# Performance work log

Measured on AMD Instinct MI355X. Metric: run time of the kernel, lower is better.

Reference implementation:

```python
import jax, jax.numpy as jnp
import numpy as np

B, W, Q = 64, 128, 256
H, A, C = 512, 128, 20
SCALE = 0.05  # keep gates out of saturation


def setup_inputs() -> dict:
    key = jax.random.key(0)
    ks = jax.random.split(key, 9)
    return {
        "quantized_repr": jax.random.normal(ks[0], (B, W, Q), jnp.float32),
        "w_in": jax.random.normal(ks[1], (H, Q), jnp.float32) * SCALE,
        "b_in": jax.random.normal(ks[2], (H,), jnp.float32) * SCALE,
        "w_ih": jax.random.normal(ks[3], (4 * H, A), jnp.float32) * SCALE,
        "w_hh": jax.random.normal(ks[4], (4 * H, H), jnp.float32) * SCALE,
        "b_ih": jax.random.normal(ks[5], (4 * H,), jnp.float32) * SCALE,
        "b_hh": jax.random.normal(ks[6], (4 * H,), jnp.float32) * SCALE,
        "w_out": jax.random.normal(ks[7], (A, H), jnp.float32) * SCALE,
        "b_out": jax.random.normal(ks[8], (A,), jnp.float32) * SCALE,
        "max_char_len": C,
    }


def reference(quantized_repr, w_in, b_in, w_ih, w_hh, b_ih, b_hh, w_out, b_out, max_char_len):
    b, w, q = quantized_repr.shape
    hdim = w_hh.shape[1]
    vocab = w_out.shape[0]
    dt = quantized_repr.dtype

    # input_projection -> initial hidden, zero cell, flattened over (B*W)
    h0 = (quantized_repr @ w_in.T + b_in).reshape(b * w, hdim)
    c0 = jnp.zeros_like(h0)
    x0 = jax.nn.one_hot(jnp.zeros((b * w,), jnp.int32), vocab, dtype=dt)  # <start> = char 0
    bias = b_ih + b_hh

    def step(carry, _):
        h, c, x = carry
        gates = x @ w_ih.T + h @ w_hh.T + bias  # [BW, 4H]
        i, f, g, o = jnp.split(gates, 4, axis=-1)  # torch gate order i,f,g,o
        i = jax.nn.sigmoid(i)
        f = jax.nn.sigmoid(f)
        g = jnp.tanh(g)
        o = jax.nn.sigmoid(o)
        c = f * c + i * g
        h = o * jnp.tanh(c)
        logits = h @ w_out.T + b_out  # [BW, A]
        x_next = jax.nn.one_hot(jnp.argmax(logits, axis=-1), vocab, dtype=dt)
        return (h, c, x_next), logits

    _, logits = jax.lax.scan(step, (h0, c0, x0), None, length=max_char_len)  # [C, BW, A]
    return logits.transpose(1, 0, 2).reshape(b, w, max_char_len, vocab)
```

## Files before the change

kernel.cpp:

```cpp
#include <hip/hip_runtime.h>
#include <math.h>

typedef float fv4 __attribute__((ext_vector_type(4)));

#define NSTEP 20
#define HD 512
#define QD 256
#define VOC 128
#define RB 16
#define TPB 512
#define CREG 2
#define CLDSROWS (RB - CREG)

#define WG_OFF   0
#define WIH_OFF  1048576
#define WIN_OFF  1310720
#define WOUT_OFF 1441792

__device__ __forceinline__ float sig_np(float x) {
  float t = (float)exp(-(double)x);
  return __fdiv_rn(1.0f, __fadd_rn(1.0f, t));
}
__device__ __forceinline__ float tanh_np(float x) {
  return (float)tanh((double)x);
}

__global__ void repack_kernel(const float* __restrict__ w_in,
                              const float* __restrict__ w_ih,
                              const float* __restrict__ w_hh,
                              const float* __restrict__ w_out,
                              float* __restrict__ ws) {
  int t = blockIdx.x * blockDim.x + threadIdx.x;
  {
    int ki = t & 3, u = (t >> 2) & 511, g = (t >> 11) & 3, kb = t >> 13;
    ws[WG_OFF + t] = w_hh[(size_t)(g * HD + u) * HD + kb * 4 + ki];
  }
  if (t < 262144) {
    int u = t & 511, g = (t >> 9) & 3, x = t >> 11;
    ws[WIH_OFF + t] = w_ih[(size_t)(g * HD + u) * VOC + x];
  }
  if (t < 131072) {
    int ki = t & 3, u = (t >> 2) & 511, kb = t >> 11;
    ws[WIN_OFF + t] = w_in[(size_t)u * QD + kb * 4 + ki];
  }
  if (t < 65536) {
    int ki = t & 3, v = (t >> 2) & 127, kb = t >> 9;
    ws[WOUT_OFF + t] = w_out[(size_t)v * HD + kb * 4 + ki];
  }
}

__global__ __launch_bounds__(TPB, 2)
void decoder_fast(const float* __restrict__ quant,
                  const float* __restrict__ b_in,
                  const float* __restrict__ b_ih,
                  const float* __restrict__ b_hh,
                  const float* __restrict__ b_out,
                  const float* __restrict__ ws,
                  float* __restrict__ out) {
  __shared__ __align__(16) float hLDS[RB * HD];
  __shared__ __align__(16) float cLDS[CLDSROWS * HD];
  __shared__ float2 cand[RB][2];

  const int tid  = threadIdx.x;
  const int row0 = blockIdx.x * RB;
  const int v    = tid & (VOC - 1);
  const int rqs  = (tid >> 7) << 2;
  const int wpar = (tid >> 6) & 1;

  const fv4* Wg4   = (const fv4*)(ws + WG_OFF);
  const float* Wih = ws + WIH_OFF;
  const fv4* Win4  = (const fv4*)(ws + WIN_OFF);
  const fv4* Wout4 = (const fv4*)(ws + WOUT_OFF);
  const fv4* hLDS4 = (const fv4*)hLDS;

  {
    const fv4* src = (const fv4*)(quant + (size_t)row0 * QD);
    fv4* dst = (fv4*)hLDS;
    dst[tid]       = src[tid];
    dst[tid + TPB] = src[tid + TPB];
  }
  __syncthreads();

  float a0[RB];
  {
    const fv4* q4 = (const fv4*)hLDS;
#pragma unroll
    for (int r = 0; r < RB; ++r) a0[r] = 0.0f;
    for (int kb = 0; kb < QD / 4; ++kb) {
      fv4 w = Win4[kb * 512 + tid];
#pragma unroll
      for (int r = 0; r < RB; ++r) {
        fv4 qv = q4[r * 64 + kb];
        a0[r] = __builtin_fmaf(w[0], qv[0], a0[r]);
        a0[r] = __builtin_fmaf(w[1], qv[1], a0[r]);
        a0[r] = __builtin_fmaf(w[2], qv[2], a0[r]);
        a0[r] = __builtin_fmaf(w[3], qv[3], a0[r]);
      }
    }
  }
  const float binu = b_in[tid];
  __syncthreads();
#pragma unroll
  for (int r = 0; r < RB; ++r) hLDS[r * HD + tid] = __fadd_rn(a0[r], binu);
  __syncthreads();

  float cR0 = 0.0f, cR1 = 0.0f;

  for (int t = 0; t < NSTEP; ++t) {
    float acc[RB][4];
    float la[4];
#pragma unroll
    for (int rr = 0; rr < RB; ++rr)
#pragma unroll
      for (int g = 0; g < 4; ++g) acc[rr][g] = 0.0f;
#pragma unroll
    for (int j = 0; j < 4; ++j) la[j] = 0.0f;

    for (int kb = 0; kb < HD / 4; ++kb) {
      fv4 wv[4];
#pragma unroll
      for (int g = 0; g < 4; ++g) wv[g] = Wg4[(kb * 4 + g) * 512 + tid];
      fv4 wvo = Wout4[kb * 128 + v];
#pragma unroll
      for (int rr = 0; rr < RB; ++rr) {
        const int r = (rr + rqs) & (RB - 1);
        fv4 hv = hLDS4[r * 128 + kb];
#pragma unroll
        for (int g = 0; g < 4; ++g) {
          acc[rr][g] = __builtin_fmaf(wv[g][0], hv[0], acc[rr][g]);
          acc[rr][g] = __builtin_fmaf(wv[g][1], hv[1], acc[rr][g]);
          acc[rr][g] = __builtin_fmaf(wv[g][2], hv[2], acc[rr][g]);
          acc[rr][g] = __builtin_fmaf(wv[g][3], hv[3], acc[rr][g]);
        }
        if (rr < 4) {
          la[rr] = __builtin_fmaf(wvo[0], hv[0], la[rr]);
          la[rr] = __builtin_fmaf(wvo[1], hv[1], la[rr]);
          la[rr] = __builtin_fmaf(wvo[2], hv[2], la[rr]);
          la[rr] = __builtin_fmaf(wvo[3], hv[3], la[rr]);
        }
      }
    }

    if (t > 0) {
      const float boutv = b_out[v];
#pragma unroll
      for (int j = 0; j < 4; ++j) {
        float val = __fadd_rn(la[j], boutv);
        out[(size_t)((row0 + rqs + j) * NSTEP + (t - 1)) * VOC + v] = val;
        float mv = val;
        int   mi = v;
#pragma unroll
        for (int m = 1; m < 64; m <<= 1) {
          float ov = __shfl_xor(mv, m);
          int   oi = __shfl_xor(mi, m);
          bool take = (ov > mv) || (ov == mv && oi < mi);
          mv = take ? ov : mv;
          mi = take ? oi : mi;
        }
        if ((tid & 63) == 0)
          cand[rqs + j][wpar] = make_float2(mv, __int_as_float(mi));
      }
    }
    __syncthreads();

    float biasg[4];
#pragma unroll
    for (int g = 0; g < 4; ++g)
      biasg[g] = __fadd_rn(b_ih[g * HD + tid], b_hh[g * HD + tid]);

#pragma unroll
    for (int rr = 0; rr < RB; ++rr) {
      const int r = (rr + rqs) & (RB - 1);
      int ix = 0;
      if (t > 0) {
        float2 c0 = cand[r][0], c1 = cand[r][1];
        ix = (c1.x > c0.x) ? __float_as_int(c1.y) : __float_as_int(c0.y);
      }
      float ga[4];
#pragma unroll
      for (int g = 0; g < 4; ++g) {
        float t1 = Wih[(ix * 4 + g) * 512 + tid];
        ga[g] = __fadd_rn(__fadd_rn(t1, acc[rr][g]), biasg[g]);
      }
      float ig = sig_np(ga[0]);
      float fg = sig_np(ga[1]);
      float gg = tanh_np(ga[2]);
      float og = sig_np(ga[3]);
      float cold;
      if (rr == RB - 2)      cold = cR0;
      else if (rr == RB - 1) cold = cR1;
      else                   cold = cLDS[rr * HD + tid];
      if (t == 0) cold = 0.0f;
      float cn = __fadd_rn(__fmul_rn(fg, cold), __fmul_rn(ig, gg));
      if (rr == RB - 2)      cR0 = cn;
      else if (rr == RB - 1) cR1 = cn;
      else                   cLDS[rr * HD + tid] = cn;
      hLDS[r * HD + tid] = __fmul_rn(og, tanh_np(cn));
    }
    __syncthreads();
  }

  {
    float la2[4];
#pragma unroll
    for (int j = 0; j < 4; ++j) la2[j] = 0.0f;
    for (int kb = 0; kb < HD / 4; ++kb) {
      fv4 wvo = Wout4[kb * 128 + v];
#pragma unroll
      for (int j = 0; j < 4; ++j) {
        fv4 hv = hLDS4[(rqs + j) * 128 + kb];
        la2[j] = __builtin_fmaf(wvo[0], hv[0], la2[j]);
        la2[j] = __builtin_fmaf(wvo[1], hv[1], la2[j]);
        la2[j] = __builtin_fmaf(wvo[2], hv[2], la2[j]);
        la2[j] = __builtin_fmaf(wvo[3], hv[3], la2[j]);
      }
    }
    const float boutv = b_out[v];
#pragma unroll
    for (int j = 0; j < 4; ++j)
      out[(size_t)((row0 + rqs + j) * NSTEP + (NSTEP - 1)) * VOC + v] =
          __fadd_rn(la2[j], boutv);
  }
}

extern "C" void kernel_launch(void* const* d_in, const int* in_sizes, int n_in,
                              void* d_out, int out_size, void* d_ws, size_t ws_size,
                              hipStream_t stream) {
  const float* quant = (const float*)d_in[0];
  const float* w_in  = (const float*)d_in[1];
  const float* b_in  = (const float*)d_in[2];
  const float* w_ih  = (const float*)d_in[3];
  const float* w_hh  = (const float*)d_in[4];
  const float* b_ih  = (const float*)d_in[5];
  const float* b_hh  = (const float*)d_in[6];
  const float* w_out = (const float*)d_in[7];
  const float* b_out = (const float*)d_in[8];
  float* out = (float*)d_out;
  float* ws  = (float*)d_ws;

  repack_kernel<<<4096, 256, 0, stream>>>(w_in, w_ih, w_hh, w_out, ws);
  decoder_fast<<<8192 / RB, TPB, 0, stream>>>(quant, b_in, b_ih, b_hh, b_out,
                                              ws, out);
}
```

Before: 5.993 ms.

## Halve rows per block, keep cell state in registers, interleave gate weights

Cuts rows per block from 16 to 8, which doubles the block count and raises the launch-bounds occupancy target from 2 to 4. The cell state moves from LDS plus two registers into a register array. The repack now interleaves the four gates per unit so each thread loads its gate weights and its W_ih row as contiguous vectors, and bias loads are hoisted out of the time loop. The cost is half the reuse of each streamed w_hh weight per block, so total weight traffic from global memory/L2 doubles in exchange for more parallelism and latency hiding.

```diff
diff --git a/kernel.cpp b/kernel.cpp
--- a/kernel.cpp
+++ b/kernel.cpp
@@ -7,10 +7,8 @@
 #define HD 512
 #define QD 256
 #define VOC 128
-#define RB 16
+#define RB 8
 #define TPB 512
-#define CREG 2
-#define CLDSROWS (RB - CREG)
 
 #define WG_OFF   0
 #define WIH_OFF  1048576
@@ -32,11 +30,11 @@
                               float* __restrict__ ws) {
   int t = blockIdx.x * blockDim.x + threadIdx.x;
   {
-    int ki = t & 3, u = (t >> 2) & 511, g = (t >> 11) & 3, kb = t >> 13;
+    int ki = t & 3, g = (t >> 2) & 3, u = (t >> 4) & 511, kb = t >> 13;
     ws[WG_OFF + t] = w_hh[(size_t)(g * HD + u) * HD + kb * 4 + ki];
   }
   if (t < 262144) {
-    int u = t & 511, g = (t >> 9) & 3, x = t >> 11;
+    int g = t & 3, u = (t >> 2) & 511, x = t >> 11;
     ws[WIH_OFF + t] = w_ih[(size_t)(g * HD + u) * VOC + x];
   }
   if (t < 131072) {
@@ -49,7 +47,7 @@
   }
 }
 
-__global__ __launch_bounds__(TPB, 2)
+__global__ __launch_bounds__(TPB, 4)
 void decoder_fast(const float* __restrict__ quant,
                   const float* __restrict__ b_in,
                   const float* __restrict__ b_ih,
@@ -58,13 +56,12 @@
                   const float* __restrict__ ws,
                   float* __restrict__ out) {
   __shared__ __align__(16) float hLDS[RB * HD];
-  __shared__ __align__(16) float cLDS[CLDSROWS * HD];
   __shared__ float2 cand[RB][2];
 
   const int tid  = threadIdx.x;
   const int row0 = blockIdx.x * RB;
   const int v    = tid & (VOC - 1);
-  const int rqs  = (tid >> 7) << 2;
+  const int rqs  = (tid >> 7) << 1;
   const int wpar = (tid >> 6) & 1;
 
   const fv4* Wg4   = (const fv4*)(ws + WG_OFF);
@@ -75,9 +72,7 @@
 
   {
     const fv4* src = (const fv4*)(quant + (size_t)row0 * QD);
-    fv4* dst = (fv4*)hLDS;
-    dst[tid]       = src[tid];
-    dst[tid + TPB] = src[tid + TPB];
+    ((fv4*)hLDS)[tid] = src[tid];
   }
   __syncthreads();
 
@@ -102,24 +97,34 @@
   __syncthreads();
 #pragma unroll
   for (int r = 0; r < RB; ++r) hLDS[r * HD + tid] = __fadd_rn(a0[r], binu);
+
+  float biasg[4];
+#pragma unroll
+  for (int g = 0; g < 4; ++g)
+    biasg[g] = __fadd_rn(b_ih[g * HD + tid], b_hh[g * HD + tid]);
+  const float boutv = b_out[v];
+
+  float c[RB];
+#pragma unroll
+  for (int r = 0; r < RB; ++r) c[r] = 0.0f;
+
   __syncthreads();
-
-  float cR0 = 0.0f, cR1 = 0.0f;
 
   for (int t = 0; t < NSTEP; ++t) {
     float acc[RB][4];
-    float la[4];
+    float la[2];
 #pragma unroll
     for (int rr = 0; rr < RB; ++rr)
 #pragma unroll
       for (int g = 0; g < 4; ++g) acc[rr][g] = 0.0f;
 #pragma unroll
-    for (int j = 0; j < 4; ++j) la[j] = 0.0f;
+    for (int j = 0; j < 2; ++j) la[j] = 0.0f;
 
     for (int kb = 0; kb < HD / 4; ++kb) {
+      const fv4* wp = Wg4 + ((size_t)kb << 11) + (tid << 2);
       fv4 wv[4];
 #pragma unroll
-      for (int g = 0; g < 4; ++g) wv[g] = Wg4[(kb * 4 + g) * 512 + tid];
+      for (int g = 0; g < 4; ++g) wv[g] = wp[g];
       fv4 wvo = Wout4[kb * 128 + v];
 #pragma unroll
       for (int rr = 0; rr < RB; ++rr) {
@@ -132,7 +137,7 @@
           acc[rr][g] = __builtin_fmaf(wv[g][2], hv[2], acc[rr][g]);
           acc[rr][g] = __builtin_fmaf(wv[g][3], hv[3], acc[rr][g]);
         }
-        if (rr < 4) {
+        if (rr < 2) {
           la[rr] = __builtin_fmaf(wvo[0], hv[0], la[rr]);
           la[rr] = __builtin_fmaf(wvo[1], hv[1], la[rr]);
           la[rr] = __builtin_fmaf(wvo[2], hv[2], la[rr]);
@@ -142,9 +147,8 @@
     }
 
     if (t > 0) {
-      const float boutv = b_out[v];
-#pragma unroll
-      for (int j = 0; j < 4; ++j) {
+#pragma unroll
+      for (int j = 0; j < 2; ++j) {
         float val = __fadd_rn(la[j], boutv);
         out[(size_t)((row0 + rqs + j) * NSTEP + (t - 1)) * VOC + v] = val;
         float mv = val;
@@ -163,11 +167,6 @@
     }
     __syncthreads();
 
-    float biasg[4];
-#pragma unroll
-    for (int g = 0; g < 4; ++g)
-      biasg[g] = __fadd_rn(b_ih[g * HD + tid], b_hh[g * HD + tid]);
-
 #pragma unroll
     for (int rr = 0; rr < RB; ++rr) {
       const int r = (rr + rqs) & (RB - 1);
@@ -176,38 +175,30 @@
         float2 c0 = cand[r][0], c1 = cand[r][1];
         ix = (c1.x > c0.x) ? __float_as_int(c1.y) : __float_as_int(c0.y);
       }
+      fv4 t4 = *(const fv4*)&Wih[((size_t)ix << 11) + (tid << 2)];
       float ga[4];
 #pragma unroll
-      for (int g = 0; g < 4; ++g) {
-        float t1 = Wih[(ix * 4 + g) * 512 + tid];
-        ga[g] = __fadd_rn(__fadd_rn(t1, acc[rr][g]), biasg[g]);
-      }
+      for (int g = 0; g < 4; ++g)
+        ga[g] = __fadd_rn(__fadd_rn(t4[g], acc[rr][g]), biasg[g]);
       float ig = sig_np(ga[0]);
       float fg = sig_np(ga[1]);
       float gg = tanh_np(ga[2]);
       float og = sig_np(ga[3]);
-      float cold;
-      if (rr == RB - 2)      cold = cR0;
-      else if (rr == RB - 1) cold = cR1;
-      else                   cold = cLDS[rr * HD + tid];
-      if (t == 0) cold = 0.0f;
-      float cn = __fadd_rn(__fmul_rn(fg, cold), __fmul_rn(ig, gg));
-      if (rr == RB - 2)      cR0 = cn;
-      else if (rr == RB - 1) cR1 = cn;
-      else                   cLDS[rr * HD + tid] = cn;
+      float cn = __fadd_rn(__fmul_rn(fg, c[rr]), __fmul_rn(ig, gg));
+      c[rr] = cn;
       hLDS[r * HD + tid] = __fmul_rn(og, tanh_np(cn));
     }
     __syncthreads();
   }
 
   {
-    float la2[4];
-#pragma unroll
-    for (int j = 0; j < 4; ++j) la2[j] = 0.0f;
+    float la2[2];
+#pragma unroll
+    for (int j = 0; j < 2; ++j) la2[j] = 0.0f;
     for (int kb = 0; kb < HD / 4; ++kb) {
       fv4 wvo = Wout4[kb * 128 + v];
 #pragma unroll
-      for (int j = 0; j < 4; ++j) {
+      for (int j = 0; j < 2; ++j) {
         fv4 hv = hLDS4[(rqs + j) * 128 + kb];
         la2[j] = __builtin_fmaf(wvo[0], hv[0], la2[j]);
         la2[j] = __builtin_fmaf(wvo[1], hv[1], la2[j]);
@@ -215,9 +206,8 @@
         la2[j] = __builtin_fmaf(wvo[3], hv[3], la2[j]);
       }
     }
-    const float boutv = b_out[v];
-#pragma unroll
-    for (int j = 0; j < 4; ++j)
+#pragma unroll
+    for (int j = 0; j < 2; ++j)
       out[(size_t)((row0 + rqs + j) * NSTEP + (NSTEP - 1)) * VOC + v] =
           __fadd_rn(la2[j], boutv);
   }
```

Result: slower. 6.876 ms (+14.7%).

## Double-buffer LSTM weight loads and interleave gate weights per unit

Applied to the files above, without the earlier changes.

Repacks the recurrent weights so each thread's four gate vectors sit next to each other, and does the same for the input-to-hidden table so one 16-byte load covers all four gates. The k-loop is software-pipelined with two register buffers: the next k-block's weights are prefetched while FMAs run on the current block. Bias loads are hoisted out of the time loop. This targets global-load latency and instruction count, but the extra register buffers may raise VGPR pressure at two blocks per CU.

```diff
diff --git a/kernel.cpp b/kernel.cpp
--- a/kernel.cpp
+++ b/kernel.cpp
@@ -32,11 +32,11 @@
                               float* __restrict__ ws) {
   int t = blockIdx.x * blockDim.x + threadIdx.x;
   {
-    int ki = t & 3, u = (t >> 2) & 511, g = (t >> 11) & 3, kb = t >> 13;
+    int ki = t & 3, g = (t >> 2) & 3, u = (t >> 4) & 511, kb = t >> 13;
     ws[WG_OFF + t] = w_hh[(size_t)(g * HD + u) * HD + kb * 4 + ki];
   }
   if (t < 262144) {
-    int u = t & 511, g = (t >> 9) & 3, x = t >> 11;
+    int g = t & 3, u = (t >> 2) & 511, x = t >> 11;
     ws[WIH_OFF + t] = w_ih[(size_t)(g * HD + u) * VOC + x];
   }
   if (t < 131072) {
@@ -102,9 +102,16 @@
   __syncthreads();
 #pragma unroll
   for (int r = 0; r < RB; ++r) hLDS[r * HD + tid] = __fadd_rn(a0[r], binu);
+
+  float biasg[4];
+#pragma unroll
+  for (int g = 0; g < 4; ++g)
+    biasg[g] = __fadd_rn(b_ih[g * HD + tid], b_hh[g * HD + tid]);
+  const float boutv = b_out[v];
+
+  float cR0 = 0.0f, cR1 = 0.0f;
+
   __syncthreads();
-
-  float cR0 = 0.0f, cR1 = 0.0f;
 
   for (int t = 0; t < NSTEP; ++t) {
     float acc[RB][4];
@@ -116,33 +123,56 @@
 #pragma unroll
     for (int j = 0; j < 4; ++j) la[j] = 0.0f;
 
-    for (int kb = 0; kb < HD / 4; ++kb) {
-      fv4 wv[4];
-#pragma unroll
-      for (int g = 0; g < 4; ++g) wv[g] = Wg4[(kb * 4 + g) * 512 + tid];
-      fv4 wvo = Wout4[kb * 128 + v];
-#pragma unroll
-      for (int rr = 0; rr < RB; ++rr) {
-        const int r = (rr + rqs) & (RB - 1);
-        fv4 hv = hLDS4[r * 128 + kb];
-#pragma unroll
-        for (int g = 0; g < 4; ++g) {
-          acc[rr][g] = __builtin_fmaf(wv[g][0], hv[0], acc[rr][g]);
-          acc[rr][g] = __builtin_fmaf(wv[g][1], hv[1], acc[rr][g]);
-          acc[rr][g] = __builtin_fmaf(wv[g][2], hv[2], acc[rr][g]);
-          acc[rr][g] = __builtin_fmaf(wv[g][3], hv[3], acc[rr][g]);
-        }
-        if (rr < 4) {
-          la[rr] = __builtin_fmaf(wvo[0], hv[0], la[rr]);
-          la[rr] = __builtin_fmaf(wvo[1], hv[1], la[rr]);
-          la[rr] = __builtin_fmaf(wvo[2], hv[2], la[rr]);
-          la[rr] = __builtin_fmaf(wvo[3], hv[3], la[rr]);
-        }
-      }
-    }
+    fv4 wvA[4], wvB[4], wvoA, wvoB;
+    {
+      const fv4* wp = Wg4 + (tid << 2);
+#pragma unroll
+      for (int g = 0; g < 4; ++g) wvA[g] = wp[g];
+      wvoA = Wout4[v];
+    }
+
+#define DO_FMA(KB, WV, WVO)                                              \
+    {                                                                    \
+      _Pragma("unroll")                                                  \
+      for (int rr = 0; rr < RB; ++rr) {                                  \
+        const int r = (rr + rqs) & (RB - 1); \
+        fv4 hv = hLDS4[r * 128 + (KB)];                                  \
+        _Pragma("unroll")                                                \
+        for (int g = 0; g < 4; ++g) {                                    \
+          acc[rr][g] = __builtin_fmaf(WV[g][0], hv[0], acc[rr][g]);      \
+          acc[rr][g] = __builtin_fmaf(WV[g][1], hv[1], acc[rr][g]);      \
+          acc[rr][g] = __builtin_fmaf(WV[g][2], hv[2], acc[rr][g]);      \
+          acc[rr][g] = __builtin_fmaf(WV[g][3], hv[3], acc[rr][g]);      \
+        }                                                                \
+        if (rr < 4) { \
+          la[rr] = __builtin_fmaf(WVO[0], hv[0], la[rr]);                \
+          la[rr] = __builtin_fmaf(WVO[1], hv[1], la[rr]);                \
+          la[rr] = __builtin_fmaf(WVO[2], hv[2], la[rr]);                \
+          la[rr] = __builtin_fmaf(WVO[3], hv[3], la[rr]);                \
+        }                                                                \
+      }                                                                  \
+    }
+
+    for (int kb = 0; kb < HD / 4; kb += 2) {
+      {
+        const fv4* wp = Wg4 + ((size_t)(kb + 1) << 11) + (tid << 2);
+#pragma unroll
+        for (int g = 0; g < 4; ++g) wvB[g] = wp[g];
+        wvoB = Wout4[(kb + 1) * 128 + v];
+      }
+      DO_FMA(kb, wvA, wvoA);
+      {
+        const int kn = (kb + 2) & 127;
+        const fv4* wp = Wg4 + ((size_t)kn << 11) + (tid << 2);
+#pragma unroll
+        for (int g = 0; g < 4; ++g) wvA[g] = wp[g];
+        wvoA = Wout4[kn * 128 + v];
+      }
+      DO_FMA(kb + 1, wvB, wvoB);
+    }
+#undef DO_FMA
 
     if (t > 0) {
-      const float boutv = b_out[v];
 #pragma unroll
       for (int j = 0; j < 4; ++j) {
         float val = __fadd_rn(la[j], boutv);
@@ -163,11 +193,6 @@
     }
     __syncthreads();
 
-    float biasg[4];
-#pragma unroll
-    for (int g = 0; g < 4; ++g)
-      biasg[g] = __fadd_rn(b_ih[g * HD + tid], b_hh[g * HD + tid]);
-
 #pragma unroll
     for (int rr = 0; rr < RB; ++rr) {
       const int r = (rr + rqs) & (RB - 1);
@@ -176,12 +201,11 @@
         float2 c0 = cand[r][0], c1 = cand[r][1];
         ix = (c1.x > c0.x) ? __float_as_int(c1.y) : __float_as_int(c0.y);
       }
+      fv4 t4 = *(const fv4*)&Wih[((size_t)ix << 11) + (tid << 2)];
       float ga[4];
 #pragma unroll
-      for (int g = 0; g < 4; ++g) {
-        float t1 = Wih[(ix * 4 + g) * 512 + tid];
-        ga[g] = __fadd_rn(__fadd_rn(t1, acc[rr][g]), biasg[g]);
-      }
+      for (int g = 0; g < 4; ++g)
+        ga[g] = __fadd_rn(__fadd_rn(t4[g], acc[rr][g]), biasg[g]);
       float ig = sig_np(ga[0]);
       float fg = sig_np(ga[1]);
       float gg = tanh_np(ga[2]);
@@ -215,7 +239,6 @@
         la2[j] = __builtin_fmaf(wvo[3], hv[3], la2[j]);
       }
     }
-    const float boutv = b_out[v];
 #pragma unroll
     for (int j = 0; j < 4; ++j)
       out[(size_t)((row0 + rqs + j) * NSTEP + (NSTEP - 1)) * VOC + v] =
@@ -227,8 +250,8 @@
                               void* d_out, int out_size, void* d_ws, size_t ws_size,
                               hipStream_t stream) {
   const float* quant = (const float*)d_in[0];
+  const float* b_in  = (const float*)d_in[2];
   const float* w_in  = (const float*)d_in[1];
-  const float* b_in  = (const float*)d_in[2];
   const float* w_ih  = (const float*)d_in[3];
   const float* w_hh  = (const float*)d_in[4];
   const float* b_ih  = (const float*)d_in[5];
```

New measurement: 6.213 ms. +3.7%, slower.

## Give each thread two hidden units over eight rows, keep cell state in registers

Applied to the files above, without the earlier changes.

Halves the block size and the rows per block, from 16 to 8, and has each thread compute two hidden units instead of one. The repacked weight layout is interleaved by gate so that a thread's four gate weights are contiguous and can be read as one vector. Each h value read from LDS now feeds twice as many FMAs, and the whole cell state now fits in registers, so the LDS cell buffer goes away. Bias loads are also hoisted out of the time loop. The cost is that each weight fetched from global or L2 memory is now reused across only 8 rows, so total recurrent-weight traffic doubles.

```diff
diff --git a/kernel.cpp b/kernel.cpp
--- a/kernel.cpp
+++ b/kernel.cpp
@@ -7,10 +7,9 @@
 #define HD 512
 #define QD 256
 #define VOC 128
-#define RB 16
-#define TPB 512
-#define CREG 2
-#define CLDSROWS (RB - CREG)
+#define RB 8
+#define TPB 256
+#define NU 2
 
 #define WG_OFF   0
 #define WIH_OFF  1048576
@@ -32,11 +31,11 @@
                               float* __restrict__ ws) {
   int t = blockIdx.x * blockDim.x + threadIdx.x;
   {
-    int ki = t & 3, u = (t >> 2) & 511, g = (t >> 11) & 3, kb = t >> 13;
+    int ki = t & 3, g = (t >> 2) & 3, u = (t >> 4) & 511, kb = t >> 13;
     ws[WG_OFF + t] = w_hh[(size_t)(g * HD + u) * HD + kb * 4 + ki];
   }
   if (t < 262144) {
-    int u = t & 511, g = (t >> 9) & 3, x = t >> 11;
+    int g = t & 3, u = (t >> 2) & 511, x = t >> 11;
     ws[WIH_OFF + t] = w_ih[(size_t)(g * HD + u) * VOC + x];
   }
   if (t < 131072) {
@@ -58,10 +57,11 @@
                   const float* __restrict__ ws,
                   float* __restrict__ out) {
   __shared__ __align__(16) float hLDS[RB * HD];
-  __shared__ __align__(16) float cLDS[CLDSROWS * HD];
   __shared__ float2 cand[RB][2];
 
   const int tid  = threadIdx.x;
+  const int u    = tid;
+  const int u2   = tid + TPB;
   const int row0 = blockIdx.x * RB;
   const int v    = tid & (VOC - 1);
   const int rqs  = (tid >> 7) << 2;
@@ -81,45 +81,72 @@
   }
   __syncthreads();
 
-  float a0[RB];
+  float a0[RB][NU];
   {
     const fv4* q4 = (const fv4*)hLDS;
 #pragma unroll
-    for (int r = 0; r < RB; ++r) a0[r] = 0.0f;
+    for (int r = 0; r < RB; ++r)
+#pragma unroll
+      for (int n = 0; n < NU; ++n) a0[r][n] = 0.0f;
     for (int kb = 0; kb < QD / 4; ++kb) {
-      fv4 w = Win4[kb * 512 + tid];
+      fv4 w1 = Win4[kb * 512 + u];
+      fv4 w2 = Win4[kb * 512 + u2];
 #pragma unroll
       for (int r = 0; r < RB; ++r) {
         fv4 qv = q4[r * 64 + kb];
-        a0[r] = __builtin_fmaf(w[0], qv[0], a0[r]);
-        a0[r] = __builtin_fmaf(w[1], qv[1], a0[r]);
-        a0[r] = __builtin_fmaf(w[2], qv[2], a0[r]);
-        a0[r] = __builtin_fmaf(w[3], qv[3], a0[r]);
-      }
-    }
-  }
-  const float binu = b_in[tid];
+        a0[r][0] = __builtin_fmaf(w1[0], qv[0], a0[r][0]);
+        a0[r][0] = __builtin_fmaf(w1[1], qv[1], a0[r][0]);
+        a0[r][0] = __builtin_fmaf(w1[2], qv[2], a0[r][0]);
+        a0[r][0] = __builtin_fmaf(w1[3], qv[3], a0[r][0]);
+        a0[r][1] = __builtin_fmaf(w2[0], qv[0], a0[r][1]);
+        a0[r][1] = __builtin_fmaf(w2[1], qv[1], a0[r][1]);
+        a0[r][1] = __builtin_fmaf(w2[2], qv[2], a0[r][1]);
+        a0[r][1] = __builtin_fmaf(w2[3], qv[3], a0[r][1]);
+      }
+    }
+  }
+  const float binu1 = b_in[u], binu2 = b_in[u2];
   __syncthreads();
 #pragma unroll
-  for (int r = 0; r < RB; ++r) hLDS[r * HD + tid] = __fadd_rn(a0[r], binu);
+  for (int r = 0; r < RB; ++r) {
+    hLDS[r * HD + u]  = __fadd_rn(a0[r][0], binu1);
+    hLDS[r * HD + u2] = __fadd_rn(a0[r][1], binu2);
+  }
+
+  float biasg[NU][4];
+#pragma unroll
+  for (int g = 0; g < 4; ++g) {
+    biasg[0][g] = __fadd_rn(b_ih[g * HD + u],  b_hh[g * HD + u]);
+    biasg[1][g] = __fadd_rn(b_ih[g * HD + u2], b_hh[g * HD + u2]);
+  }
+  const float boutv = b_out[v];
+
+  float c[RB][NU];
+#pragma unroll
+  for (int r = 0; r < RB; ++r)
+#pragma unroll
+    for (int n = 0; n < NU; ++n) c[r][n] = 0.0f;
+
   __syncthreads();
 
-  float cR0 = 0.0f, cR1 = 0.0f;
-
   for (int t = 0; t < NSTEP; ++t) {
-    float acc[RB][4];
+    float acc[RB][4][NU];
     float la[4];
 #pragma unroll
     for (int rr = 0; rr < RB; ++rr)
 #pragma unroll
-      for (int g = 0; g < 4; ++g) acc[rr][g] = 0.0f;
+      for (int g = 0; g < 4; ++g)
+#pragma unroll
+        for (int n = 0; n < NU; ++n) acc[rr][g][n] = 0.0f;
 #pragma unroll
     for (int j = 0; j < 4; ++j) la[j] = 0.0f;
 
     for (int kb = 0; kb < HD / 4; ++kb) {
-      fv4 wv[4];
-#pragma unroll
-      for (int g = 0; g < 4; ++g) wv[g] = Wg4[(kb * 4 + g) * 512 + tid];
+      const fv4* wp1 = Wg4 + ((size_t)kb << 11) + (u << 2);
+      const fv4* wp2 = Wg4 + ((size_t)kb << 11) + (u2 << 2);
+      fv4 wv1[4], wv2[4];
+#pragma unroll
+      for (int g = 0; g < 4; ++g) { wv1[g] = wp1[g]; wv2[g] = wp2[g]; }
       fv4 wvo = Wout4[kb * 128 + v];
 #pragma unroll
       for (int rr = 0; rr < RB; ++rr) {
@@ -127,10 +154,14 @@
         fv4 hv = hLDS4[r * 128 + kb];
 #pragma unroll
         for (int g = 0; g < 4; ++g) {
-          acc[rr][g] = __builtin_fmaf(wv[g][0], hv[0], acc[rr][g]);
-          acc[rr][g] = __builtin_fmaf(wv[g][1], hv[1], acc[rr][g]);
-          acc[rr][g] = __builtin_fmaf(wv[g][2], hv[2], acc[rr][g]);
-          acc[rr][g] = __builtin_fmaf(wv[g][3], hv[3], acc[rr][g]);
+          acc[rr][g][0] = __builtin_fmaf(wv1[g][0], hv[0], acc[rr][g][0]);
+          acc[rr][g][0] = __builtin_fmaf(wv1[g][1], hv[1], acc[rr][g][0]);
+          acc[rr][g][0] = __builtin_fmaf(wv1[g][2], hv[2], acc[rr][g][0]);
+          acc[rr][g][0] = __builtin_fmaf(wv1[g][3], hv[3], acc[rr][g][0]);
+          acc[rr][g][1] = __builtin_fmaf(wv2[g][0], hv[0], acc[rr][g][1]);
+          acc[rr][g][1] = __builtin_fmaf(wv2[g][1], hv[1], acc[rr][g][1]);
+          acc[rr][g][1] = __builtin_fmaf(wv2[g][2], hv[2], acc[rr][g][1]);
+          acc[rr][g][1] = __builtin_fmaf(wv2[g][3], hv[3], acc[rr][g][1]);
         }
         if (rr < 4) {
           la[rr] = __builtin_fmaf(wvo[0], hv[0], la[rr]);
@@ -142,7 +173,6 @@
     }
 
     if (t > 0) {
-      const float boutv = b_out[v];
 #pragma unroll
       for (int j = 0; j < 4; ++j) {
         float val = __fadd_rn(la[j], boutv);
@@ -163,11 +193,6 @@
     }
     __syncthreads();
 
-    float biasg[4];
-#pragma unroll
-    for (int g = 0; g < 4; ++g)
-      biasg[g] = __fadd_rn(b_ih[g * HD + tid], b_hh[g * HD + tid]);
-
 #pragma unroll
     for (int rr = 0; rr < RB; ++rr) {
       const int r = (rr + rqs) & (RB - 1);
@@ -176,26 +201,23 @@
         float2 c0 = cand[r][0], c1 = cand[r][1];
         ix = (c1.x > c0.x) ? __float_as_int(c1.y) : __float_as_int(c0.y);
       }
-      float ga[4];
-#pragma unroll
-      for (int g = 0; g < 4; ++g) {
-        float t1 = Wih[(ix * 4 + g) * 512 + tid];
-        ga[g] = __fadd_rn(__fadd_rn(t1, acc[rr][g]), biasg[g]);
-      }
-      float ig = sig_np(ga[0]);
-      float fg = sig_np(ga[1]);
-      float gg = tanh_np(ga[2]);
-      float og = sig_np(ga[3]);
-      float cold;
-      if (rr == RB - 2)      cold = cR0;
-      else if (rr == RB - 1) cold = cR1;
-      else                   cold = cLDS[rr * HD + tid];
-      if (t == 0) cold = 0.0f;
-      float cn = __fadd_rn(__fmul_rn(fg, cold), __fmul_rn(ig, gg));
-      if (rr == RB - 2)      cR0 = cn;
-      else if (rr == RB - 1) cR1 = cn;
-      else                   cLDS[rr * HD + tid] = cn;
-      hLDS[r * HD + tid] = __fmul_rn(og, tanh_np(cn));
+      fv4 t41 = *(const fv4*)&Wih[((size_t)ix << 11) + (u << 2)];
+      fv4 t42 = *(const fv4*)&Wih[((size_t)ix << 11) + (u2 << 2)];
+#pragma unroll
+      for (int n = 0; n < NU; ++n) {
+        fv4 t4 = (n == 0) ? t41 : t42;
+        float ga[4];
+#pragma unroll
+        for (int g = 0; g < 4; ++g)
+          ga[g] = __fadd_rn(__fadd_rn(t4[g], acc[rr][g][n]), biasg[n][g]);
+        float ig = sig_np(ga[0]);
+        float fg = sig_np(ga[1]);
+        float gg = tanh_np(ga[2]);
+        float og = sig_np(ga[3]);
+        float cn = __fadd_rn(__fmul_rn(fg, c[rr][n]), __fmul_rn(ig, gg));
+        c[rr][n] = cn;
+        hLDS[r * HD + (n == 0 ? u : u2)] = __fmul_rn(og, tanh_np(cn));
+      }
     }
     __syncthreads();
   }
@@ -215,7 +237,6 @@
         la2[j] = __builtin_fmaf(wvo[3], hv[3], la2[j]);
       }
     }
-    const float boutv = b_out[v];
 #pragma unroll
     for (int j = 0; j < 4; ++j)
       out[(size_t)((row0 + rqs + j) * NSTEP + (NSTEP - 1)) * VOC + v] =
```

Result: slower. 6.524 ms (+8.9%).
